# Performance work log

Hardware: AMD Instinct MI355X
Metric: run time of the kernel (lower is better)

## Reference

```python
import jax, jax.numpy as jnp
import numpy as np

B, C, H, W = 16, 512, 32, 32
NH = 8
HD = C // NH  # 64


def setup_inputs() -> dict:
    key = jax.random.key(0)
    ks = jax.random.split(key, 9)
    s = 1.0 / np.sqrt(C)
    return {
        "x": jax.random.normal(ks[0], (B, C, H, W), dtype=jnp.float32),
        "Wq": jax.random.normal(ks[1], (C, C), dtype=jnp.float32) * s,
        "bq": jnp.zeros((C,), dtype=jnp.float32),
        "Wk": jax.random.normal(ks[2], (C, C), dtype=jnp.float32) * s,
        "bk": jnp.zeros((C,), dtype=jnp.float32),
        "Wv": jax.random.normal(ks[3], (C, C), dtype=jnp.float32) * s,
        "bv": jnp.zeros((C,), dtype=jnp.float32),
        "Wo": jax.random.normal(ks[4], (C, C), dtype=jnp.float32) * s,
        "bo": jnp.zeros((C,), dtype=jnp.float32),
    }


def reference(x, Wq, bq, Wk, bk, Wv, bv, Wo, bo):
    b, c, h, w = x.shape
    n = h * w  # sequence of spatial tokens
    # [B, C, H, W] -> [B, N, C]
    xf = x.reshape(b, c, n).transpose(0, 2, 1)
    # separate QKV projections, split heads: [B, NH, N, HD]
    def split_heads(t):
        return t.reshape(b, n, NH, HD).transpose(0, 2, 1, 3)
    q = split_heads(xf @ Wq + bq)
    k = split_heads(xf @ Wk + bk)
    v = split_heads(xf @ Wv + bv)
    # energy: [B, NH, N, N]
    energy = jnp.einsum('bhqd,bhkd->bhqk', q, k) / jnp.sqrt(jnp.float32(HD))
    attn = jax.nn.softmax(energy, axis=-1)
    out = jnp.einsum('bhqk,bhkd->bhqd', attn, v)  # [B, NH, N, HD]
    out = out.transpose(0, 2, 1, 3).reshape(b, n, c)
    out = out @ Wo + bo
    return out.transpose(0, 2, 1).reshape(b, c, h, w)
```

## Files before the change

### kernel.cpp

```cpp
#include <hip/hip_runtime.h>
#include <hip/hip_bf16.h>
#include <math.h>

constexpr int B_  = 16;
constexpr int C_  = 512;
constexpr int N_  = 1024;
constexpr int NH_ = 8;
constexpr int HD_ = 64;

#define QSCALE 0.18033688f

typedef __attribute__((ext_vector_type(8))) short short8;
typedef __attribute__((ext_vector_type(4))) short short4v;
typedef __attribute__((ext_vector_type(4))) float f32x4;
typedef __attribute__((ext_vector_type(2))) int int2v;
#define MFMA16(a, b, c) __builtin_amdgcn_mfma_f32_16x16x32_bf16((a), (b), (c), 0, 0, 0)

#if __has_builtin(__builtin_amdgcn_exp2f)
#define EXP2(x) __builtin_amdgcn_exp2f(x)
#else
#define EXP2(x) exp2f(x)
#endif

__device__ __forceinline__ short f2bf(float f) {
    union { float f; unsigned u; } a; a.f = f;
    unsigned r = a.u + 0x7fffu + ((a.u >> 16) & 1u);
    return (short)(r >> 16);
}
__device__ __forceinline__ short f2bf_hw(float f) {
    __hip_bfloat16 h = __float2bfloat16(f);
    return *reinterpret_cast<short*>(&h);
}

__device__ __forceinline__ void gload_lds16(const void* g, void* l) {
    __builtin_amdgcn_global_load_lds(
        (const __attribute__((address_space(1))) unsigned*)g,
        (__attribute__((address_space(3))) unsigned*)l, 16, 0, 0);
}

__device__ __forceinline__ float xor32_add(float x) {
#if __has_builtin(__builtin_amdgcn_permlane32_swap)
    int2v p = __builtin_amdgcn_permlane32_swap(__float_as_int(x), __float_as_int(x), false, false);
    return __int_as_float(p[0]) + __int_as_float(p[1]);
#else
    return x + __shfl_xor(x, 32);
#endif
}

__global__ __launch_bounds__(256) void prep_x(const float* __restrict__ x,
                                              short* __restrict__ xt) {
    const int wgid = blockIdx.x;
    const int xcd = wgid & 7;
    const int i = wgid >> 3;
    const int b  = 2 * xcd + (i >= 128);
    const int tile = i & 127;
    const int tn = tile >> 3;
    const int tc = tile & 7;
    __shared__ float t[64][65];
    const int tid = threadIdx.x;
    #pragma unroll
    for (int k = 0; k < 16; ++k) {
        int idx = k * 256 + tid;
        int r = idx >> 6, col = idx & 63;
        t[r][col] = x[((size_t)b * C_ + tc * 64 + r) * N_ + tn * 64 + col];
    }
    __syncthreads();
    #pragma unroll
    for (int k = 0; k < 16; ++k) {
        int idx = k * 256 + tid;
        int r2 = idx >> 6, col2 = idx & 63;
        xt[((size_t)b * N_ + tn * 64 + r2) * C_ + tc * 64 + col2] = f2bf(t[col2][r2]);
    }
}

__global__ __launch_bounds__(256) void prep_w(
    const float* __restrict__ Wq, const float* __restrict__ Wk,
    const float* __restrict__ Wv, const float* __restrict__ Wo,
    short* __restrict__ WqT, short* __restrict__ WkT,
    short* __restrict__ WvT, short* __restrict__ WoT) {
    const int z = blockIdx.y;
    const float* W = (z == 0) ? Wq : (z == 1) ? Wk : (z == 2) ? Wv : Wo;
    short* WT      = (z == 0) ? WqT : (z == 1) ? WkT : (z == 2) ? WvT : WoT;
    const int tco = blockIdx.x / (C_ / 64);
    const int tc  = blockIdx.x % (C_ / 64);
    __shared__ float t[64][65];
    const int tid = threadIdx.x;
    #pragma unroll
    for (int i = 0; i < 16; ++i) {
        int idx = i * 256 + tid;
        int r = idx >> 6, col = idx & 63;
        t[r][col] = W[((size_t)tc * 64 + r) * C_ + tco * 64 + col];
    }
    __syncthreads();
    #pragma unroll
    for (int i = 0; i < 16; ++i) {
        int idx = i * 256 + tid;
        int r2 = idx >> 6, col2 = idx & 63;
        WT[((size_t)tco * 64 + r2) * C_ + tc * 64 + col2] = f2bf(t[col2][r2]);
    }
}

#define GEMM_STAGE(buf, t)                                                    \
    {                                                                         \
        _Pragma("unroll")                                                     \
        for (int ii = 0; ii < 4; ++ii) {                                      \
            gload_lds16(Ag + arowoff + (size_t)ii * 8 * C_ + (t) * 64,        \
                        &smem[buf][0][wave * 32 + ii * 8][0]);                \
            gload_lds16(Bg + arowoff + (size_t)ii * 8 * C_ + (t) * 64,        \
                        &smem[buf][1][wave * 32 + ii * 8][0]);                \
        }                                                                     \
    }

#define GEMM_CORE()                                                           \
    GEMM_STAGE(0, 0);                                                         \
    __syncthreads();                                                          \
    for (int t = 0; t < 8; ++t) {                                             \
        const int buf = t & 1;                                                \
        if (t < 7) GEMM_STAGE(buf ^ 1, t + 1);                                \
        __builtin_amdgcn_s_setprio(1);                                        \
        _Pragma("unroll")                                                     \
        for (int ks = 0; ks < 2; ++ks) {                                      \
            short8 af[4], bf[4];                                              \
            const int sw = ((ks * 4 + g) ^ (c & 7)) << 3;                     \
            _Pragma("unroll")                                                 \
            for (int fm = 0; fm < 4; ++fm)                                    \
                af[fm] = *(const short8*)&smem[buf][0][wm * 64 + fm * 16 + c][sw]; \
            _Pragma("unroll")                                                 \
            for (int fn = 0; fn < 4; ++fn)                                    \
                bf[fn] = *(const short8*)&smem[buf][1][wn * 64 + fn * 16 + c][sw]; \
            _Pragma("unroll")                                                 \
            for (int fm = 0; fm < 4; ++fm)                                    \
                _Pragma("unroll")                                             \
                for (int fn = 0; fn < 4; ++fn)                                \
                    acc[fm][fn] = MFMA16(af[fm], bf[fn], acc[fm][fn]);        \
        }                                                                     \
        __builtin_amdgcn_s_setprio(0);                                        \
        __syncthreads();                                                      \
    }

__global__ __launch_bounds__(256) void qkv_mfma(
    const short* __restrict__ xt,
    const short* __restrict__ WqT, const float* __restrict__ bq,
    const short* __restrict__ WkT, const float* __restrict__ bk,
    const short* __restrict__ WvT, const float* __restrict__ bv,
    short* __restrict__ Qs, short* __restrict__ Kb, short* __restrict__ Vt) {
    const int wgid = blockIdx.x;
    const int xcd = wgid & 7;
    const int i = wgid >> 3;
    const int b = 2 * xcd + (i >= 96);
    const int rem = (i >= 96) ? i - 96 : i;
    const int z = rem >> 5;
    const int tile = rem & 31;
    const int mt = tile >> 2;
    const int nt = tile & 3;
    const int tid = threadIdx.x;
    const int wave = tid >> 6, lane = tid & 63;
    const int g = lane >> 4, c = lane & 15;
    const int wm = wave >> 1, wn = wave & 1;

    const short* W    = (z == 0) ? WqT : (z == 1) ? WkT : WvT;
    const float* bias = (z == 0) ? bq  : (z == 1) ? bk  : bv;

    __shared__ __align__(16) short smem[2][2][128][64];

    const short* Ag = xt + (size_t)b * N_ * C_ + (size_t)mt * 128 * C_;
    const short* Bg = W + (size_t)nt * 128 * C_;

    const int lrow = lane >> 3, lslot = lane & 7;
    const size_t arowoff = (size_t)(wave * 32 + lrow) * C_ + ((lslot ^ lrow) << 3);

    f32x4 acc[4][4] = {};
    GEMM_CORE();

    const int tok0 = mt * 128 + wm * 64;
    const int co0  = nt * 128 + wn * 64;
    const int h = co0 >> 6;
    const size_t bh = (size_t)(b * NH_ + h);

    if (z < 2) {
        short* Y = (z == 0) ? Qs : Kb;
        const float sc = (z == 0) ? QSCALE : 1.f;
        #pragma unroll
        for (int fm = 0; fm < 4; ++fm)
            #pragma unroll
            for (int fn = 0; fn < 4; ++fn)
                #pragma unroll
                for (int r = 0; r < 4; ++r) {
                    int tok = tok0 + fm * 16 + 4 * g + r;
                    int hd  = fn * 16 + c;
                    float v = (acc[fm][fn][r] + bias[co0 + hd]) * sc;
                    Y[(bh * N_ + tok) * HD_ + hd] = f2bf_hw(v);
                }
    } else {
        short (*t72)[72] = (short(*)[72])((short*)smem + wave * 32 * 72);
        #pragma unroll
        for (int p = 0; p < 2; ++p) {
            #pragma unroll
            for (int fn2 = 0; fn2 < 2; ++fn2) {
                int fnn = 2 * p + fn2;
                #pragma unroll
                for (int fm = 0; fm < 4; ++fm) {
                    short4v pk;
                    #pragma unroll
                    for (int r = 0; r < 4; ++r)
                        pk[r] = f2bf_hw(acc[fm][fnn][r] + bias[co0 + fnn * 16 + c]);
                    *(short4v*)&t72[fn2 * 16 + c][fm * 16 + 4 * g] = pk;
                }
            }
            int row = lane >> 1, half2 = lane & 1;
            int hd = p * 32 + row;
            size_t base = (bh * HD_ + hd) * N_ + tok0 + half2 * 32;
            #pragma unroll
            for (int j = 0; j < 4; ++j)
                *(short8*)&Vt[base + j * 8] = *(const short8*)&t72[row][half2 * 32 + j * 8];
        }
    }
}

__global__ __launch_bounds__(256) void attn_mfma(
    const short* __restrict__ Qs, const short* __restrict__ Kb,
    const short* __restrict__ Vt, short* __restrict__ Ah) {
    const int wgid = blockIdx.x;
    const int swz  = (wgid & 7) * 128 + (wgid >> 3);
    const int b  = swz >> 6;
    const int h  = (swz >> 3) & 7;
    const int qt = swz & 7;
    const int tid = threadIdx.x;
    const int wave = tid >> 6, lane = tid & 63;
    const int g = lane >> 4, c = lane & 15;
    const int q0 = qt * 128 + wave * 32;
    const size_t bh = (size_t)(b * NH_ + h);

    const short* Qw  = Qs + (bh * N_ + q0) * HD_;
    const short* Kbb = Kb + bh * N_ * HD_;
    const short* Vtb = Vt + bh * HD_ * N_;

    __shared__ short KV[2][2][4096];
    __shared__ short Pl[4][32][72];
    short (*P)[72] = Pl[wave];

    const int srow = tid >> 3;
    const int sc16 = tid & 7;
    const int sswz = 8 * (sc16 ^ (srow & 7));
    const int kdst0 = srow * 64 + sswz;
    const int kdst1 = (srow + 32) * 64 + sswz;
    short8 gk0, gk1, gv0, gv1;

    #define STAGE_LOAD(key0)                                                   \
        do {                                                                   \
            gk0 = *(const short8*)&Kbb[(size_t)((key0) + srow) * HD_ + sc16 * 8];      \
            gk1 = *(const short8*)&Kbb[(size_t)((key0) + srow + 32) * HD_ + sc16 * 8]; \
            gv0 = *(const short8*)&Vtb[(size_t)srow * N_ + (key0) + sc16 * 8];         \
            gv1 = *(const short8*)&Vtb[(size_t)(srow + 32) * N_ + (key0) + sc16 * 8];  \
        } while (0)
    #define STAGE_WRITE(buf)                                                   \
        do {                                                                   \
            *(short8*)&KV[buf][0][kdst0] = gk0;                                \
            *(short8*)&KV[buf][0][kdst1] = gk1;                                \
            *(short8*)&KV[buf][1][kdst0] = gv0;                                \
            *(short8*)&KV[buf][1][kdst1] = gv1;                                \
        } while (0)

    short8 qf[2][2];
    #pragma unroll
    for (int f = 0; f < 2; ++f)
        #pragma unroll
        for (int k0 = 0; k0 < 2; ++k0)
            qf[f][k0] = *(const short8*)&Qw[(f * 16 + c) * HD_ + k0 * 32 + g * 8];

    f32x4 o[2][4] = {};
    float lpart[2] = {0.f, 0.f};

    STAGE_LOAD(0);
    STAGE_WRITE(0);
    STAGE_LOAD(64);
    __syncthreads();

    int cur = 0;
    for (int it = 0; it < 16; ++it) {
        if (it < 15) STAGE_WRITE(cur ^ 1);
        if (it < 14) STAGE_LOAD((it + 2) * 64);

        const short* Kl = &KV[cur][0][0];
        const short* Vl = &KV[cur][1][0];

        f32x4 s[2][4] = {};
        __builtin_amdgcn_s_setprio(1);
        #pragma unroll
        for (int m = 0; m < 4; ++m) {
            const int row = m * 16 + c;
            short8 ka = *(const short8*)&Kl[row * 64 + 8 * ((g)     ^ (row & 7))];
            short8 kb = *(const short8*)&Kl[row * 64 + 8 * ((4 + g) ^ (row & 7))];
            s[0][m] = MFMA16(ka, qf[0][0], s[0][m]);
            s[0][m] = MFMA16(kb, qf[0][1], s[0][m]);
            s[1][m] = MFMA16(ka, qf[1][0], s[1][m]);
            s[1][m] = MFMA16(kb, qf[1][1], s[1][m]);
        }
        __builtin_amdgcn_s_setprio(0);

        #pragma unroll
        for (int f = 0; f < 2; ++f) {
            float ps[2] = {0.f, 0.f};
            #pragma unroll
            for (int m = 0; m < 4; ++m) {
                #pragma unroll
                for (int r = 0; r < 4; ++r) {
                    float p = EXP2(s[f][m][r]);
                    s[f][m][r] = p;
                    ps[m & 1] += p;
                }
            }
            lpart[f] += ps[0] + ps[1];
            #pragma unroll
            for (int m = 0; m < 4; ++m) {
                short4v pk;
                #pragma unroll
                for (int r = 0; r < 4; ++r) pk[r] = f2bf_hw(s[f][m][r]);
                *(short4v*)&P[f * 16 + c][m * 16 + 4 * g] = pk;
            }
        }

        short8 pa[2][2];
        #pragma unroll
        for (int f = 0; f < 2; ++f)
            #pragma unroll
            for (int k0 = 0; k0 < 2; ++k0)
                pa[f][k0] = *(const short8*)&P[f * 16 + c][k0 * 32 + g * 8];
        __builtin_amdgcn_s_setprio(1);
        #pragma unroll
        for (int n = 0; n < 4; ++n) {
            const int row = n * 16 + c;
            short8 va = *(const short8*)&Vl[row * 64 + 8 * ((g)     ^ (row & 7))];
            short8 vb = *(const short8*)&Vl[row * 64 + 8 * ((4 + g) ^ (row & 7))];
            o[0][n] = MFMA16(pa[0][0], va, o[0][n]);
            o[0][n] = MFMA16(pa[0][1], vb, o[0][n]);
            o[1][n] = MFMA16(pa[1][0], va, o[1][n]);
            o[1][n] = MFMA16(pa[1][1], vb, o[1][n]);
        }
        __builtin_amdgcn_s_setprio(0);

        __syncthreads();
        cur ^= 1;
    }
    #undef STAGE_LOAD
    #undef STAGE_WRITE

    #pragma unroll
    for (int f = 0; f < 2; ++f) {
        float l = lpart[f];
        l += __shfl_xor(l, 16);
        l = xor32_add(l);
        float li[4];
        #pragma unroll
        for (int r = 0; r < 4; ++r) li[r] = 1.f / __shfl(l, 4 * g + r);
        #pragma unroll
        for (int n = 0; n < 4; ++n)
            #pragma unroll
            for (int r = 0; r < 4; ++r) {
                int tok = q0 + f * 16 + 4 * g + r;
                int cc  = h * 64 + n * 16 + c;
                Ah[((size_t)b * N_ + tok) * C_ + cc] = f2bf_hw(o[f][n][r] * li[r]);
            }
    }
}

__global__ __launch_bounds__(256) void proj_mfma(
    const short* __restrict__ Ah, const short* __restrict__ WoT,
    const float* __restrict__ bo, float* __restrict__ out) {
    const int wgid = blockIdx.x;
    const int xcd = wgid & 7;
    const int i = wgid >> 3;
    const int b = 2 * xcd + (i >= 32);
    const int tile = i & 31;
    const int mt = tile >> 2;
    const int nt = tile & 3;
    const int tid = threadIdx.x;
    const int wave = tid >> 6, lane = tid & 63;
    const int g = lane >> 4, c = lane & 15;
    const int wm = wave >> 1, wn = wave & 1;

    __shared__ __align__(16) short smem[2][2][128][64];

    const short* Ag = Ah + (size_t)b * N_ * C_ + (size_t)mt * 128 * C_;
    const short* Bg = WoT + (size_t)nt * 128 * C_;

    const int lrow = lane >> 3, lslot = lane & 7;
    const size_t arowoff = (size_t)(wave * 32 + lrow) * C_ + ((lslot ^ lrow) << 3);

    f32x4 acc[4][4] = {};
    GEMM_CORE();

    const int tok0 = mt * 128 + wm * 64;
    const int co0  = nt * 128 + wn * 64;

    float (*tf)[68] = (float(*)[68])((float*)smem + wave * 32 * 68);
    #pragma unroll
    for (int p = 0; p < 2; ++p) {
        #pragma unroll
        for (int fm = 0; fm < 4; ++fm)
            #pragma unroll
            for (int fn2 = 0; fn2 < 2; ++fn2) {
                float4 v = *(float4*)&acc[fm][2 * p + fn2];
                *(float4*)&tf[fn2 * 16 + c][fm * 16 + 4 * g] = v;
            }
        int row = lane >> 1, half = lane & 1;
        int co = co0 + p * 32 + row;
        float bias = bo[co];
        float* ob = out + ((size_t)b * C_ + co) * N_ + tok0 + half * 32;
        #pragma unroll
        for (int j = 0; j < 8; ++j) {
            float4 v = *(const float4*)&tf[row][half * 32 + j * 4];
            v.x += bias; v.y += bias; v.z += bias; v.w += bias;
            *(float4*)&ob[j * 4] = v;
        }
    }
}

extern "C" void kernel_launch(void* const* d_in, const int* in_sizes, int n_in,
                              void* d_out, int out_size, void* d_ws, size_t ws_size,
                              hipStream_t stream) {
    (void)in_sizes; (void)n_in; (void)out_size; (void)ws_size;
    const float* x  = (const float*)d_in[0];
    const float* Wq = (const float*)d_in[1];
    const float* bq = (const float*)d_in[2];
    const float* Wk = (const float*)d_in[3];
    const float* bk = (const float*)d_in[4];
    const float* Wv = (const float*)d_in[5];
    const float* bv = (const float*)d_in[6];
    const float* Wo = (const float*)d_in[7];
    const float* bo = (const float*)d_in[8];
    float* out = (float*)d_out;

    char* ws = (char*)d_ws;
    const size_t MB = 1024 * 1024;
    short* xt  = (short*)(ws + 0 * MB);
    short* WqT = (short*)(ws + 16 * MB);
    short* WkT = (short*)(ws + 16 * MB + 512 * 1024);
    short* WvT = (short*)(ws + 17 * MB);
    short* WoT = (short*)(ws + 17 * MB + 512 * 1024);
    short* Qsb = (short*)(ws + 18 * MB);
    short* Kb  = (short*)(ws + 34 * MB);
    short* Vt  = (short*)(ws + 50 * MB);
    short* Ah  = (short*)(ws + 66 * MB);

    prep_x<<<dim3(2048), 256, 0, stream>>>(x, xt);
    prep_w<<<dim3(64, 4), 256, 0, stream>>>(Wq, Wk, Wv, Wo, WqT, WkT, WvT, WoT);
    qkv_mfma<<<dim3(1536), 256, 0, stream>>>(xt, WqT, bq, WkT, bk, WvT, bv,
                                             Qsb, Kb, Vt);
    attn_mfma<<<dim3(1024), 256, 0, stream>>>(Qsb, Kb, Vt, Ah);
    proj_mfma<<<dim3(512), 256, 0, stream>>>(Ah, WoT, bo, out);
}
```

Measured before the change: 124.3 us.

## Widen attention blocks to 8 waves, compute row sums via MFMA, swizzle P

The attention kernel now runs 512-thread blocks covering 256 queries, so each K/V tile staged in LDS is shared by twice as many waves, and each thread loads only one K and one V vector per stage. The softmax row sums are computed by an extra MFMA of the bf16 P tile against a ones vector, which replaces the per-element float adds and the cross-lane shuffles. The P scratch buffer drops its padding in favour of an XOR swizzle to avoid LDS bank conflicts. Risks include lower occupancy from larger blocks with fewer of them, and row sums taken from bf16-rounded probabilities.

```diff
diff --git a/kernel.cpp b/kernel.cpp
--- a/kernel.cpp
+++ b/kernel.cpp
@@ -13,7 +13,6 @@
 typedef __attribute__((ext_vector_type(8))) short short8;
 typedef __attribute__((ext_vector_type(4))) short short4v;
 typedef __attribute__((ext_vector_type(4))) float f32x4;
-typedef __attribute__((ext_vector_type(2))) int int2v;
 #define MFMA16(a, b, c) __builtin_amdgcn_mfma_f32_16x16x32_bf16((a), (b), (c), 0, 0, 0)
 
 #if __has_builtin(__builtin_amdgcn_exp2f)
@@ -36,15 +35,6 @@
     __builtin_amdgcn_global_load_lds(
         (const __attribute__((address_space(1))) unsigned*)g,
         (__attribute__((address_space(3))) unsigned*)l, 16, 0, 0);
-}
-
-__device__ __forceinline__ float xor32_add(float x) {
-#if __has_builtin(__builtin_amdgcn_permlane32_swap)
-    int2v p = __builtin_amdgcn_permlane32_swap(__float_as_int(x), __float_as_int(x), false, false);
-    return __int_as_float(p[0]) + __int_as_float(p[1]);
-#else
-    return x + __shfl_xor(x, 32);
-#endif
 }
 
 __global__ __launch_bounds__(256) void prep_x(const float* __restrict__ x,
@@ -217,18 +207,18 @@
     }
 }
 
-__global__ __launch_bounds__(256) void attn_mfma(
+__global__ __launch_bounds__(512) void attn_mfma(
     const short* __restrict__ Qs, const short* __restrict__ Kb,
     const short* __restrict__ Vt, short* __restrict__ Ah) {
     const int wgid = blockIdx.x;
-    const int swz  = (wgid & 7) * 128 + (wgid >> 3);
-    const int b  = swz >> 6;
-    const int h  = (swz >> 3) & 7;
-    const int qt = swz & 7;
+    const int swz  = (wgid & 7) * 64 + (wgid >> 3);
+    const int b  = swz >> 5;
+    const int h  = (swz >> 2) & 7;
+    const int qt = swz & 3;
     const int tid = threadIdx.x;
     const int wave = tid >> 6, lane = tid & 63;
     const int g = lane >> 4, c = lane & 15;
-    const int q0 = qt * 128 + wave * 32;
+    const int q0 = qt * 256 + wave * 32;
     const size_t bh = (size_t)(b * NH_ + h);
 
     const short* Qw  = Qs + (bh * N_ + q0) * HD_;
@@ -236,29 +226,24 @@
     const short* Vtb = Vt + bh * HD_ * N_;
 
     __shared__ short KV[2][2][4096];
-    __shared__ short Pl[4][32][72];
-    short (*P)[72] = Pl[wave];
+    __shared__ short Pl[8][32][64];
+    short (*P)[64] = Pl[wave];
+    const int px = (c & 7) << 1;
 
     const int srow = tid >> 3;
     const int sc16 = tid & 7;
-    const int sswz = 8 * (sc16 ^ (srow & 7));
-    const int kdst0 = srow * 64 + sswz;
-    const int kdst1 = (srow + 32) * 64 + sswz;
-    short8 gk0, gk1, gv0, gv1;
+    const int kdst = srow * 64 + 8 * (sc16 ^ (srow & 7));
+    short8 gk, gv;
 
     #define STAGE_LOAD(key0)                                                   \
         do {                                                                   \
-            gk0 = *(const short8*)&Kbb[(size_t)((key0) + srow) * HD_ + sc16 * 8];      \
-            gk1 = *(const short8*)&Kbb[(size_t)((key0) + srow + 32) * HD_ + sc16 * 8]; \
-            gv0 = *(const short8*)&Vtb[(size_t)srow * N_ + (key0) + sc16 * 8];         \
-            gv1 = *(const short8*)&Vtb[(size_t)(srow + 32) * N_ + (key0) + sc16 * 8];  \
+            gk = *(const short8*)&Kbb[(size_t)((key0) + srow) * HD_ + sc16 * 8]; \
+            gv = *(const short8*)&Vtb[(size_t)srow * N_ + (key0) + sc16 * 8];    \
         } while (0)
     #define STAGE_WRITE(buf)                                                   \
         do {                                                                   \
-            *(short8*)&KV[buf][0][kdst0] = gk0;                                \
-            *(short8*)&KV[buf][0][kdst1] = gk1;                                \
-            *(short8*)&KV[buf][1][kdst0] = gv0;                                \
-            *(short8*)&KV[buf][1][kdst1] = gv1;                                \
+            *(short8*)&KV[buf][0][kdst] = gk;                                  \
+            *(short8*)&KV[buf][1][kdst] = gv;                                  \
         } while (0)
 
     short8 qf[2][2];
@@ -268,8 +253,12 @@
         for (int k0 = 0; k0 < 2; ++k0)
             qf[f][k0] = *(const short8*)&Qw[(f * 16 + c) * HD_ + k0 * 32 + g * 8];
 
+    short8 ones8;
+    #pragma unroll
+    for (int j = 0; j < 8; ++j) ones8[j] = (short)0x3F80;
+
     f32x4 o[2][4] = {};
-    float lpart[2] = {0.f, 0.f};
+    f32x4 lacc[2] = {};
 
     STAGE_LOAD(0);
     STAGE_WRITE(0);
@@ -300,23 +289,12 @@
 
         #pragma unroll
         for (int f = 0; f < 2; ++f) {
-            float ps[2] = {0.f, 0.f};
-            #pragma unroll
-            for (int m = 0; m < 4; ++m) {
-                #pragma unroll
-                for (int r = 0; r < 4; ++r) {
-                    float p = EXP2(s[f][m][r]);
-                    s[f][m][r] = p;
-                    ps[m & 1] += p;
-                }
-            }
-            lpart[f] += ps[0] + ps[1];
             #pragma unroll
             for (int m = 0; m < 4; ++m) {
                 short4v pk;
                 #pragma unroll
-                for (int r = 0; r < 4; ++r) pk[r] = f2bf_hw(s[f][m][r]);
-                *(short4v*)&P[f * 16 + c][m * 16 + 4 * g] = pk;
+                for (int r = 0; r < 4; ++r) pk[r] = f2bf_hw(EXP2(s[f][m][r]));
+                *(short4v*)&P[f * 16 + c][((4 * m + g) ^ px) * 4] = pk;
             }
         }
 
@@ -325,8 +303,12 @@
         for (int f = 0; f < 2; ++f)
             #pragma unroll
             for (int k0 = 0; k0 < 2; ++k0)
-                pa[f][k0] = *(const short8*)&P[f * 16 + c][k0 * 32 + g * 8];
+                pa[f][k0] = *(const short8*)&P[f * 16 + c][((k0 * 8 + 2 * g) ^ px) * 4];
         __builtin_amdgcn_s_setprio(1);
+        lacc[0] = MFMA16(pa[0][0], ones8, lacc[0]);
+        lacc[0] = MFMA16(pa[0][1], ones8, lacc[0]);
+        lacc[1] = MFMA16(pa[1][0], ones8, lacc[1]);
+        lacc[1] = MFMA16(pa[1][1], ones8, lacc[1]);
         #pragma unroll
         for (int n = 0; n < 4; ++n) {
             const int row = n * 16 + c;
@@ -347,12 +329,9 @@
 
     #pragma unroll
     for (int f = 0; f < 2; ++f) {
-        float l = lpart[f];
-        l += __shfl_xor(l, 16);
-        l = xor32_add(l);
         float li[4];
         #pragma unroll
-        for (int r = 0; r < 4; ++r) li[r] = 1.f / __shfl(l, 4 * g + r);
+        for (int r = 0; r < 4; ++r) li[r] = 1.f / lacc[f][r];
         #pragma unroll
         for (int n = 0; n < 4; ++n)
             #pragma unroll
@@ -447,6 +426,6 @@
     prep_w<<<dim3(64, 4), 256, 0, stream>>>(Wq, Wk, Wv, Wo, WqT, WkT, WvT, WoT);
     qkv_mfma<<<dim3(1536), 256, 0, stream>>>(xt, WqT, bq, WkT, bk, WvT, bv,
                                              Qsb, Kb, Vt);
-    attn_mfma<<<dim3(1024), 256, 0, stream>>>(Qsb, Kb, Vt, Ah);
+    attn_mfma<<<dim3(512), 512, 0, stream>>>(Qsb, Kb, Vt, Ah);
     proj_mfma<<<dim3(512), 256, 0, stream>>>(Ah, WoT, bo, out);
 }
```

Measured after the change: 110.8 us. 10.9% less time.
